# Optimization experiments

Hardware: AMD Instinct MI355X
Metric: run time of the kernel (lower is better)

## Reference

```python
import jax, jax.numpy as jnp
import numpy as np

PI_2 = 3.14159 / 2  # matches the torch module's pi_2 constant
EPS = 1e-8          # F.cosine_similarity default eps


def setup_inputs() -> dict:
    key = jax.random.key(0)
    k1, k2 = jax.random.split(key)
    B, N, C, H, W = 32, 2000, 512, 7, 7
    key_t = jax.random.normal(k1, (B, C, H, W), dtype=jnp.float32)
    memory = jax.random.normal(k2, (N, C, H, W), dtype=jnp.float32)
    return {"key": key_t, "memory": memory}


def reference(key, memory):
    # Memory.read(key): cosine-similarity addressing + tan warp + softmax, then weighted read.
    B = key.shape[0]
    N = memory.shape[0]
    k = key.reshape(B, -1)        # [B, D], D = C*H*W
    m = memory.reshape(N, -1)     # [N, D]
    # cosine similarity with torch's eps clamping on norms
    dots = jnp.einsum('bd,nd->bn', k, m)                                   # [B, N]
    k_norm = jnp.maximum(jnp.sqrt(jnp.sum(k * k, axis=-1, keepdims=True)), EPS)  # [B, 1]
    m_norm = jnp.maximum(jnp.sqrt(jnp.sum(m * m, axis=-1)), EPS)                 # [N]
    cos = dots / (k_norm * m_norm[None, :])                                 # [B, N]
    w = jax.nn.softmax(jnp.tan(cos * PI_2), axis=1)                         # [B, N]
    # weighted read: sum_n w[b,n] * memory[n,c,h,w] -> [B, C, H, W]
    out = jnp.einsum('bn,nchw->bchw', w, memory)
    return out
```

## Files before the change

kernel.cpp:

```cpp
#include <hip/hip_runtime.h>
#include <math.h>

#define D_ELEMS 25088
#define D4      6272
#define N_MEM   2000
#define B_KEYS  32
#define PI_2F   1.570795f
#define EPSF    1e-8f
#define NSLICE  49
#define KSLICE  512
#define KSTEPS  16
#define NTILE   250

using short8 = __attribute__((ext_vector_type(8))) short;
using short4v = __attribute__((ext_vector_type(4))) short;
using f32x4  = __attribute__((ext_vector_type(4))) float;


__device__ inline short f2bf(float x) {
    union { float f; unsigned u; } v; v.f = x;
    unsigned r = v.u + 0x7fffu + ((v.u >> 16) & 1u);
    return (short)(r >> 16);
}

__global__ __launch_bounds__(256) void k_prep(const float* __restrict__ key,
                                              short* __restrict__ keyb,
                                              float* __restrict__ knorm) {
    const int b   = blockIdx.x;
    const int tid = threadIdx.x;
    const float4* K4 = (const float4*)(key + (size_t)b * D_ELEMS);
    short4v* KB4 = (short4v*)keyb + (size_t)b * D4;
    float ks = 0.f;
    for (int i = tid; i < D4; i += 256) {
        const float4 f = K4[i];
        short4v s;
        s[0] = f2bf(f.x); s[1] = f2bf(f.y); s[2] = f2bf(f.z); s[3] = f2bf(f.w);
        KB4[i] = s;
        ks += f.x * f.x + f.y * f.y + f.z * f.z + f.w * f.w;
    }
#pragma unroll
    for (int o = 1; o < 64; o <<= 1) ks += __shfl_xor(ks, o, 64);
    __shared__ float sred[4];
    if ((tid & 63) == 0) sred[tid >> 6] = ks;
    __syncthreads();
    if (tid == 0)
        knorm[b] = fmaxf(sqrtf(sred[0] + sred[1] + sred[2] + sred[3]), EPSF);
}

__global__ __launch_bounds__(64) void k_dots_mfma(const short* __restrict__ keyb,
                                                  const float* __restrict__ mem,
                                                  float* __restrict__ dots_part,
                                                  float* __restrict__ mn2_part) {
    const int nt   = blockIdx.x / NSLICE;
    const int s    = blockIdx.x % NSLICE;
    const int n0   = nt * 16;
    const int lane = threadIdx.x;
    const int quad = lane >> 4;
    const int l16  = lane & 15;
    const int k0   = s * KSLICE + quad * 8;

    const short* a0p = keyb + (size_t)l16 * D_ELEMS + k0;
    const short* a1p = keyb + (size_t)(16 + l16) * D_ELEMS + k0;
    const float4* bp = (const float4*)(mem + (size_t)(n0 + l16) * D_ELEMS + k0);

    f32x4 acc0 = {0.f, 0.f, 0.f, 0.f};
    f32x4 acc1 = {0.f, 0.f, 0.f, 0.f};
    float msq = 0.f;

    short8 a0 = *(const short8*)a0p;
    short8 a1 = *(const short8*)a1p;
    float4 f0 = bp[0], f1 = bp[1];

    for (int t = 0; t < KSTEPS; ++t) {
        const short8 a0c = a0, a1c = a1;
        const float4 f0c = f0, f1c = f1;
        if (t + 1 < KSTEPS) {
            a0 = *(const short8*)(a0p + (t + 1) * 32);
            a1 = *(const short8*)(a1p + (t + 1) * 32);
            f0 = bp[(t + 1) * 8];
            f1 = bp[(t + 1) * 8 + 1];
        }
        msq += f0c.x * f0c.x + f0c.y * f0c.y + f0c.z * f0c.z + f0c.w * f0c.w
             + f1c.x * f1c.x + f1c.y * f1c.y + f1c.z * f1c.z + f1c.w * f1c.w;
        short8 b;
        b[0] = f2bf(f0c.x); b[1] = f2bf(f0c.y); b[2] = f2bf(f0c.z); b[3] = f2bf(f0c.w);
        b[4] = f2bf(f1c.x); b[5] = f2bf(f1c.y); b[6] = f2bf(f1c.z); b[7] = f2bf(f1c.w);
        acc0 = __builtin_amdgcn_mfma_f32_16x16x32_bf16(a0c, b, acc0, 0, 0, 0);
        acc1 = __builtin_amdgcn_mfma_f32_16x16x32_bf16(a1c, b, acc1, 0, 0, 0);
    }

    float* dp = dots_part + (size_t)(s * N_MEM + n0 + l16) * B_KEYS;
#pragma unroll
    for (int r = 0; r < 4; ++r) {
        dp[quad * 4 + r]      = acc0[r];
        dp[16 + quad * 4 + r] = acc1[r];
    }

    msq += __shfl_xor(msq, 16, 64);
    msq += __shfl_xor(msq, 32, 64);
    if (lane < 16) mn2_part[s * N_MEM + n0 + lane] = msq;
}

__global__ __launch_bounds__(256) void k_reduce(const float* __restrict__ dots_part,
                                                const float* __restrict__ mn2_part,
                                                float* __restrict__ dots,
                                                float* __restrict__ mn2) {
    const int gid = blockIdx.x * 256 + threadIdx.x;
    float ds = 0.f;
#pragma unroll
    for (int s = 0; s < NSLICE; ++s) ds += dots_part[s * (N_MEM * B_KEYS) + gid];
    dots[gid] = ds;
    if (gid < N_MEM) {
        float ms = 0.f;
#pragma unroll
        for (int s = 0; s < NSLICE; ++s) ms += mn2_part[s * N_MEM + gid];
        mn2[gid] = ms;
    }
}

__global__ __launch_bounds__(512) void k_softmax(const float* __restrict__ knormArr,
                                                 const float* __restrict__ dots,
                                                 const float* __restrict__ mn2,
                                                 float* __restrict__ w) {
    const int b   = blockIdx.x;
    const int tid = threadIdx.x;
    __shared__ float sred[512];
    __shared__ float xbuf[N_MEM];
    const float knorm = knormArr[b];

    float mx = -1e30f;
    for (int n = tid; n < N_MEM; n += 512) {
        const float mn = fmaxf(sqrtf(mn2[n]), EPSF);
        const float x  = __tanf((dots[n * B_KEYS + b] / (knorm * mn)) * PI_2F);
        xbuf[n] = x;
        mx = fmaxf(mx, x);
    }
    sred[tid] = mx;
    __syncthreads();
    for (int o = 256; o; o >>= 1) {
        if (tid < o) sred[tid] = fmaxf(sred[tid], sred[tid + o]);
        __syncthreads();
    }
    mx = sred[0];
    __syncthreads();

    float sm = 0.f;
    for (int n = tid; n < N_MEM; n += 512) {
        const float e = __expf(xbuf[n] - mx);
        xbuf[n] = e;
        sm += e;
    }
    sred[tid] = sm;
    __syncthreads();
    for (int o = 256; o; o >>= 1) {
        if (tid < o) sred[tid] += sred[tid + o];
        __syncthreads();
    }
    const float inv = 1.f / sred[0];

    for (int n = tid; n < N_MEM; n += 512)
        w[n * B_KEYS + b] = xbuf[n] * inv;
}

__global__ __launch_bounds__(256, 4) void k_read(const float* __restrict__ mem,
                                                 const float* __restrict__ w,
                                                 float* __restrict__ partial,
                                                 int nPerS) {
    const int db   = blockIdx.x % 98;
    const int s    = blockIdx.x / 98;
    const int n0   = s * nPerS;
    const int bg   = threadIdx.x >> 6;
    const int lane = threadIdx.x & 63;
    const int d4   = db * 64 + lane;

    const float4* M4 = (const float4*)mem;
    const float4* W4 = (const float4*)w;
    __shared__ float4 wls4[NTILE * 8];

    float acc[8][4];
#pragma unroll
    for (int i = 0; i < 8; ++i)
#pragma unroll
        for (int j = 0; j < 4; ++j) acc[i][j] = 0.f;

    for (int c0 = 0; c0 < nPerS; c0 += NTILE) {
        __syncthreads();
        for (int i = threadIdx.x; i < NTILE * 8; i += 256)
            wls4[i] = W4[(size_t)(n0 + c0) * 8 + i];
        __syncthreads();

        const float4* mp = M4 + (size_t)(n0 + c0) * D4 + d4;
#pragma unroll 5
        for (int nn = 0; nn < NTILE; ++nn) {
            const float4 mc = mp[(size_t)nn * D4];
            const float4 wa = wls4[nn * 8 + bg * 2];
            const float4 wb = wls4[nn * 8 + bg * 2 + 1];
            const float wv[8] = {wa.x, wa.y, wa.z, wa.w, wb.x, wb.y, wb.z, wb.w};
#pragma unroll
            for (int i = 0; i < 8; ++i) {
                acc[i][0] += wv[i] * mc.x;
                acc[i][1] += wv[i] * mc.y;
                acc[i][2] += wv[i] * mc.z;
                acc[i][3] += wv[i] * mc.w;
            }
        }
    }

    float4* P4 = (float4*)partial;
#pragma unroll
    for (int i = 0; i < 8; ++i)
        P4[(size_t)(s * B_KEYS + bg * 8 + i) * D4 + d4] =
            make_float4(acc[i][0], acc[i][1], acc[i][2], acc[i][3]);
}

__global__ __launch_bounds__(256) void k_finish(const float* __restrict__ partial,
                                                float* __restrict__ out, int ns) {
    const int i = blockIdx.x * 256 + threadIdx.x;
    const float4* P4 = (const float4*)partial;
    float4 sum = P4[i];
    for (int s = 1; s < ns; ++s) {
        const float4 p = P4[(size_t)s * (B_KEYS * D4) + i];
        sum.x += p.x; sum.y += p.y; sum.z += p.z; sum.w += p.w;
    }
    ((float4*)out)[i] = sum;
}

extern "C" void kernel_launch(void* const* d_in, const int* in_sizes, int n_in,
                              void* d_out, int out_size, void* d_ws, size_t ws_size,
                              hipStream_t stream) {
    (void)in_sizes; (void)n_in; (void)out_size;
    const float* key = (const float*)d_in[0];
    const float* mem = (const float*)d_in[1];
    float* out = (float*)d_out;
    float* ws  = (float*)d_ws;

    short* keyb      = (short*)ws;
    float* dots_part = ws + 401408;
    float* mn2_part  = ws + 3537408;
    float* dots      = ws + 3635408;
    float* mn2       = ws + 3699408;
    float* knorm     = ws + 3701408;
    float* w         = ws + 3701440;
    float* part      = ws + 3765440;

    int ns = 8;
    while (ns > 1 && (size_t)(3765440 + (size_t)ns * 802816) * 4 > ws_size) ns >>= 1;
    const int nPerS = N_MEM / ns;

    k_prep     <<<B_KEYS, 256, 0, stream>>>(key, keyb, knorm);
    k_dots_mfma<<<125 * NSLICE, 64, 0, stream>>>(keyb, mem, dots_part, mn2_part);
    k_reduce   <<<250, 256, 0, stream>>>(dots_part, mn2_part, dots, mn2);
    k_softmax  <<<B_KEYS, 512, 0, stream>>>(knorm, dots, mn2, w);
    k_read     <<<98 * ns, 256, 0, stream>>>(mem, w, part, nPerS);
    k_finish   <<<784, 256, 0, stream>>>(part, out, ns);
}
```

Measured before the change: 375.5 us.

## Stage memory tiles through LDS in k_read and split key prep kernel

k_read previously had each of the four waves load the same memory row from global memory. It now stages a 25-row memory tile cooperatively into shared memory, so each row is fetched from global once per block and then read by all four waves. Separately, key bf16 conversion moves to a wide 784-block kernel, and the key norm computation goes to its own 32-block kernel. The trade-offs are more barriers per small tile, no overlap of loads with compute, and one extra kernel launch.

```diff
diff --git a/kernel.cpp b/kernel.cpp
--- a/kernel.cpp
+++ b/kernel.cpp
@@ -10,7 +10,7 @@
 #define NSLICE  49
 #define KSLICE  512
 #define KSTEPS  16
-#define NTILE   250
+#define MTILE   25
 
 using short8 = __attribute__((ext_vector_type(8))) short;
 using short4v = __attribute__((ext_vector_type(4))) short;
@@ -24,18 +24,21 @@
 }
 
 __global__ __launch_bounds__(256) void k_prep(const float* __restrict__ key,
-                                              short* __restrict__ keyb,
-                                              float* __restrict__ knorm) {
+                                              short* __restrict__ keyb) {
+    const int i = blockIdx.x * 256 + threadIdx.x;
+    const float4 f = ((const float4*)key)[i];
+    short4v s; s[0] = f2bf(f.x); s[1] = f2bf(f.y); s[2] = f2bf(f.z); s[3] = f2bf(f.w);
+    ((short4v*)keyb)[i] = s;
+}
+
+__global__ __launch_bounds__(256) void k_knorm(const float* __restrict__ key,
+                                               float* __restrict__ knorm) {
     const int b   = blockIdx.x;
     const int tid = threadIdx.x;
     const float4* K4 = (const float4*)(key + (size_t)b * D_ELEMS);
-    short4v* KB4 = (short4v*)keyb + (size_t)b * D4;
     float ks = 0.f;
     for (int i = tid; i < D4; i += 256) {
         const float4 f = K4[i];
-        short4v s;
-        s[0] = f2bf(f.x); s[1] = f2bf(f.y); s[2] = f2bf(f.z); s[3] = f2bf(f.w);
-        KB4[i] = s;
         ks += f.x * f.x + f.y * f.y + f.z * f.z + f.w * f.w;
     }
 #pragma unroll
@@ -169,39 +172,42 @@
     const int db   = blockIdx.x % 98;
     const int s    = blockIdx.x / 98;
     const int n0   = s * nPerS;
-    const int bg   = threadIdx.x >> 6;
     const int lane = threadIdx.x & 63;
+    const int wv   = threadIdx.x >> 6;
     const int d4   = db * 64 + lane;
 
     const float4* M4 = (const float4*)mem;
     const float4* W4 = (const float4*)w;
-    __shared__ float4 wls4[NTILE * 8];
+
+    __shared__ float4 mls[MTILE * 64];
+    __shared__ float4 wls[MTILE * 8];
 
     float acc[8][4];
 #pragma unroll
-    for (int i = 0; i < 8; ++i)
-#pragma unroll
-        for (int j = 0; j < 4; ++j) acc[i][j] = 0.f;
-
-    for (int c0 = 0; c0 < nPerS; c0 += NTILE) {
-        __syncthreads();
-        for (int i = threadIdx.x; i < NTILE * 8; i += 256)
-            wls4[i] = W4[(size_t)(n0 + c0) * 8 + i];
-        __syncthreads();
-
-        const float4* mp = M4 + (size_t)(n0 + c0) * D4 + d4;
+    for (int i = 0; i < 8; ++i) {
+        acc[i][0] = 0.f; acc[i][1] = 0.f; acc[i][2] = 0.f; acc[i][3] = 0.f;
+    }
+
+    for (int c0 = 0; c0 < nPerS; c0 += MTILE) {
+        __syncthreads();
+        for (int i = threadIdx.x; i < MTILE * 64; i += 256)
+            mls[i] = M4[(size_t)(n0 + c0 + (i >> 6)) * D4 + db * 64 + (i & 63)];
+        if (threadIdx.x < MTILE * 8)
+            wls[threadIdx.x] = W4[(size_t)(n0 + c0) * 8 + threadIdx.x];
+        __syncthreads();
+
 #pragma unroll 5
-        for (int nn = 0; nn < NTILE; ++nn) {
-            const float4 mc = mp[(size_t)nn * D4];
-            const float4 wa = wls4[nn * 8 + bg * 2];
-            const float4 wb = wls4[nn * 8 + bg * 2 + 1];
-            const float wv[8] = {wa.x, wa.y, wa.z, wa.w, wb.x, wb.y, wb.z, wb.w};
+        for (int r = 0; r < MTILE; ++r) {
+            const float4 mc = mls[r * 64 + lane];
+            const float4 wa = wls[r * 8 + wv * 2];
+            const float4 wb = wls[r * 8 + wv * 2 + 1];
+            const float wvv[8] = {wa.x, wa.y, wa.z, wa.w, wb.x, wb.y, wb.z, wb.w};
 #pragma unroll
             for (int i = 0; i < 8; ++i) {
-                acc[i][0] += wv[i] * mc.x;
-                acc[i][1] += wv[i] * mc.y;
-                acc[i][2] += wv[i] * mc.z;
-                acc[i][3] += wv[i] * mc.w;
+                acc[i][0] += wvv[i] * mc.x;
+                acc[i][1] += wvv[i] * mc.y;
+                acc[i][2] += wvv[i] * mc.z;
+                acc[i][3] += wvv[i] * mc.w;
             }
         }
     }
@@ -209,7 +215,7 @@
     float4* P4 = (float4*)partial;
 #pragma unroll
     for (int i = 0; i < 8; ++i)
-        P4[(size_t)(s * B_KEYS + bg * 8 + i) * D4 + d4] =
+        P4[(size_t)(s * B_KEYS + wv * 8 + i) * D4 + d4] =
             make_float4(acc[i][0], acc[i][1], acc[i][2], acc[i][3]);
 }
 
@@ -247,7 +253,8 @@
     while (ns > 1 && (size_t)(3765440 + (size_t)ns * 802816) * 4 > ws_size) ns >>= 1;
     const int nPerS = N_MEM / ns;
 
-    k_prep     <<<B_KEYS, 256, 0, stream>>>(key, keyb, knorm);
+    k_prep     <<<784, 256, 0, stream>>>(key, keyb);
+    k_knorm    <<<B_KEYS, 256, 0, stream>>>(key, knorm);
     k_dots_mfma<<<125 * NSLICE, 64, 0, stream>>>(keyb, mem, dots_part, mn2_part);
     k_reduce   <<<250, 256, 0, stream>>>(dots_part, mn2_part, dots, mn2);
     k_softmax  <<<B_KEYS, 512, 0, stream>>>(knorm, dots, mn2, w);
```

Result: no change. 373.2 us (-0.6%).
